# Kernel optimization log

Measured on AMD Instinct MI355X. Metric: run time of the kernel, lower is better.

## Reference

```python
import jax, jax.numpy as jnp
import numpy as np


def setup_inputs() -> dict:
    key = jax.random.key(0)
    k1, k2, k3, k4 = jax.random.split(key, 4)
    B, Cin, H, W = 16, 64, 96, 96
    D, O, KH, KW, S = 100, 256, 3, 3, 3
    x = jax.random.normal(k1, (B, Cin, H, W), dtype=jnp.float32)
    dictionary = jax.random.normal(k2, (D, Cin, KH, KW), dtype=jnp.float32) * 0.05
    lookup_coefficients = jax.random.normal(k3, (O, KH, KW, S), dtype=jnp.float32) * 0.1
    lookup_indices = jax.random.randint(k4, (O, KH, KW, S), 0, D, dtype=jnp.int64)
    return {
        "x": x,
        "dictionary": dictionary,
        "lookup_coefficients": lookup_coefficients,
        "lookup_indices": lookup_indices,
    }


def reference(x, dictionary, lookup_coefficients, lookup_indices):
    # Dense conv with the small dictionary: [B, Cin, H, W] x [D, Cin, kh, kw] -> [B, D, Oh, Ow]
    conv_out = jax.lax.conv_general_dilated(
        x, dictionary,
        window_strides=(1, 1),
        padding=((1, 1), (1, 1)),
        dimension_numbers=("NCHW", "OIHW", "NCHW"),
    )
    O = lookup_coefficients.shape[0]
    D = dictionary.shape[0]
    # Flatten kernel-position and sparsity axes: each (position, slot) contributes
    # coeff * conv_out[:, idx] to output channel o; COO duplicates sum.
    idx = lookup_indices.reshape(O, -1)      # [O, P*S]
    coeff = lookup_coefficients.reshape(O, -1)  # [O, P*S]
    # Scatter-add into a per-output-channel weight over dictionary entries: W[o, d]
    Wmat = jnp.zeros((O, D), dtype=conv_out.dtype).at[jnp.arange(O)[:, None], idx].add(coeff)
    # Gather-weighted-sum == sparse (O x D) matmul against conv_out channels
    out = jnp.einsum("od,bdhw->bohw", Wmat, conv_out)
    return out
```

## Files before the change

kernel.cpp:

```cpp
#include <hip/hip_runtime.h>

#define NB   16
#define CIN  64
#define HH   96
#define WW   96
#define DD   100
#define OO   256
#define NWG  (NB * HH)
#define NCV  1536
#define WPAD 50

typedef __attribute__((ext_vector_type(8))) short  bf16x8;
typedef __attribute__((ext_vector_type(4))) float  f32x4;

#define FSWZ(wp) ((((wp) ^ ((wp) >> 3)) & 7) << 4)

static __device__ __forceinline__ unsigned short f32_to_bf16(float f) {
    unsigned int u = __float_as_uint(f);
    u += 0x7FFFu + ((u >> 16) & 1u);
    return (unsigned short)(u >> 16);
}

__global__ __launch_bounds__(256) void prep_kernel(
    const float* __restrict__ x, const float* __restrict__ dict,
    const float* __restrict__ coeff, const int* __restrict__ idx,
    unsigned short* __restrict__ x2, unsigned short* __restrict__ weff2,
    unsigned short* __restrict__ zbuf)
{
    __shared__ unsigned short lds[CIN * 100];
    __shared__ float wrow[DD];
    const int blk = blockIdx.x, tid = threadIdx.x;

    if (blk < NWG) {
        const int b = blk / HH, h = blk % HH;
        for (int it = 0; it < 6; ++it) {
            int i = tid + it * 256;
            int c = i / 24, w4 = i % 24;
            float4 v = *reinterpret_cast<const float4*>(
                x + (((size_t)(b * CIN + c) * HH + h) * WW + w4 * 4));
            ushort4 u;
            u.x = f32_to_bf16(v.x); u.y = f32_to_bf16(v.y);
            u.z = f32_to_bf16(v.z); u.w = f32_to_bf16(v.w);
            *reinterpret_cast<ushort4*>(&lds[c * 100 + w4 * 4]) = u;
        }
        __syncthreads();
        for (int it = 0; it < 6; ++it) {
            int i = tid + it * 256;
            int w = i / 16, c = (i % 16) * 4;
            ushort4 u;
            u.x = lds[(c + 0) * 100 + w];
            u.y = lds[(c + 1) * 100 + w];
            u.z = lds[(c + 2) * 100 + w];
            u.w = lds[(c + 3) * 100 + w];
            *reinterpret_cast<ushort4*>(x2 + (((size_t)(b * HH + h) * WW + w) * CIN + c)) = u;
        }
    } else {
        const int o = blk - NWG;
        if (o == 0 && tid < 8) zbuf[tid] = 0;
        if (tid < DD) wrow[tid] = 0.f;
        __syncthreads();
        if (tid == 0) {
            for (int s = 0; s < 27; ++s) wrow[idx[o * 27 + s]] += coeff[o * 27 + s];
        }
        __syncthreads();
        for (int j = tid; j < 576; j += 256) {
            int kpos = j >> 6, c = j & 63;
            float s = 0.f;
            for (int d = 0; d < DD; ++d)
                s += wrow[d] * dict[d * 576 + c * 9 + kpos];
            int otile = o >> 4, ks = c >> 5;
            int lane8 = (o & 15) | (((c >> 3) & 3) << 4);
            weff2[((size_t)(kpos * 32 + otile * 2 + ks)) * 512 + lane8 * 8 + (c & 7)]
                = f32_to_bf16(s);
        }
    }
}

__global__ __launch_bounds__(256, 2) void conv_kernel(
    const unsigned short* __restrict__ x2,
    const unsigned short* __restrict__ weff2,
    const unsigned short* __restrict__ zbuf,
    float* __restrict__ out)
{
    __shared__ unsigned short xs[4 * WPAD * 64];

    const int wg  = blockIdx.x;
    const int swz = (wg & 7) * (NCV / 8) + (wg >> 3);
    const int b = swz / 96, rem = swz % 96;
    const int hp = rem >> 1, wh = rem & 1;
    const int h0 = hp * 2, ws = wh * 48;
    const int tid = threadIdx.x;
    const int lane = tid & 63, wn = tid >> 6;
    const int l15 = lane & 15;

    char* xsb = reinterpret_cast<char*>(xs);
    const char* x2b = reinterpret_cast<const char*>(x2) + (size_t)b * HH * WW * 128;
    const char* zbp = reinterpret_cast<const char*>(zbuf);

    const unsigned short* wbase = weff2 + (size_t)(wn * 8) * 512 + lane * 8;
    bf16x8 bfr[4][4];
#pragma unroll
    for (int s = 0; s < 4; ++s) {
        const int off = (s >> 1) * 32 + (s & 1);
#pragma unroll
        for (int n = 0; n < 4; ++n)
            bfr[s][n] = *reinterpret_cast<const bf16x8*>(wbase + (off + n * 2) * 512);
    }

#pragma unroll
    for (int it = 0; it < 7; ++it) {
        int chunk = tid + it * 256;
        if (chunk < 1600) {
            int r = chunk / 400, rem2 = chunk % 400;
            int wp = rem2 >> 3, gb = (rem2 & 7) << 4;
            int hx = h0 - 1 + r, w = ws - 1 + wp;
            const char* src = (w >= 0 && w < WW && hx >= 0 && hx < HH)
                ? x2b + ((size_t)(hx * WW + w) * 128 + (gb ^ FSWZ(wp)))
                : zbp;
            __builtin_amdgcn_global_load_lds(
                (const __attribute__((address_space(1))) void*)src,
                (__attribute__((address_space(3))) void*)(xsb + chunk * 16),
                16, 0, 0);
        }
    }

    f32x4 acc[2][3][4];
#pragma unroll
    for (int q = 0; q < 2; ++q)
#pragma unroll
        for (int m = 0; m < 3; ++m)
#pragma unroll
            for (int n = 0; n < 4; ++n)
                acc[q][m][n] = (f32x4){0.f, 0.f, 0.f, 0.f};

    __syncthreads();

    bf16x8 ax[2][2][3];
    {
        const int cb0 = ((lane >> 4) * 8) * 2;
#pragma unroll
        for (int q = 0; q < 2; ++q)
#pragma unroll
            for (int m = 0; m < 3; ++m) {
                int wpos = m * 16 + l15;
                ax[0][q][m] = *reinterpret_cast<const bf16x8*>(
                    xsb + q * 6400 + wpos * 128 + (cb0 ^ FSWZ(wpos)));
            }
    }

#pragma unroll
    for (int s = 0; s < 18; ++s) {
        if (s < 17) {
            const int s1 = s + 1;
            const int kpos1 = s1 >> 1, ks1 = s1 & 1;
            const int kh1 = kpos1 / 3, dw1 = kpos1 % 3;
            const int cb1 = (ks1 * 32 + (lane >> 4) * 8) * 2;
#pragma unroll
            for (int q = 0; q < 2; ++q)
#pragma unroll
                for (int m = 0; m < 3; ++m) {
                    int wpos = m * 16 + l15 + dw1;
                    ax[s1 & 1][q][m] = *reinterpret_cast<const bf16x8*>(
                        xsb + (kh1 + q) * 6400 + wpos * 128 + (cb1 ^ FSWZ(wpos)));
                }
        }
        __builtin_amdgcn_s_setprio(1);
#pragma unroll
        for (int q = 0; q < 2; ++q)
#pragma unroll
            for (int m = 0; m < 3; ++m)
#pragma unroll
                for (int n = 0; n < 4; ++n)
                    acc[q][m][n] = __builtin_amdgcn_mfma_f32_16x16x32_bf16(
                        ax[s & 1][q][m], bfr[s & 3][n], acc[q][m][n], 0, 0, 0);
        __builtin_amdgcn_s_setprio(0);
        if (s < 14) {
            const int s4 = s + 4;
            const int off = (s4 >> 1) * 32 + (s4 & 1);
#pragma unroll
            for (int n = 0; n < 4; ++n)
                bfr[s & 3][n] = *reinterpret_cast<const bf16x8*>(
                    wbase + (off + n * 2) * 512);
        }
    }

#pragma unroll
    for (int q = 0; q < 2; ++q)
#pragma unroll
        for (int m = 0; m < 3; ++m)
#pragma unroll
            for (int n = 0; n < 4; ++n) {
                int o = wn * 64 + n * 16 + l15;
                int w = ws + m * 16 + (lane >> 4) * 4;
                *reinterpret_cast<f32x4*>(
                    out + (((size_t)(b * OO + o) * HH + h0 + q) * WW + w))
                    = acc[q][m][n];
            }
}

extern "C" void kernel_launch(void* const* d_in, const int* in_sizes, int n_in,
                              void* d_out, int out_size, void* d_ws, size_t ws_size,
                              hipStream_t stream) {
    const float* x     = (const float*)d_in[0];
    const float* dict  = (const float*)d_in[1];
    const float* coeff = (const float*)d_in[2];
    const int*   idx   = (const int*)d_in[3];
    float* out = (float*)d_out;

    char* ws = (char*)d_ws;
    unsigned short* weff2 = (unsigned short*)ws;
    unsigned short* zbuf  = (unsigned short*)(ws + 294912);
    unsigned short* x2    = (unsigned short*)(ws + 1048576);

    prep_kernel<<<NWG + OO, 256, 0, stream>>>(x, dict, coeff, idx, x2, weff2, zbuf);
    conv_kernel<<<NCV, 256, 0, stream>>>(x2, weff2, zbuf, out);
}
```

Baseline: 68.69 us.

## Fuse fp32-to-bf16 input conversion and transpose into conv kernel

Removes the separate prep pass that wrote a bf16 NHWC copy of x to workspace. Each conv workgroup now loads its fp32 rows (with halo) directly, converts them to bf16 into an LDS staging buffer, then transposes into the swizzled channel-last tile. The weight-prep kernel becomes a standalone small launch. This avoids the intermediate global write and re-read, but costs more LDS per block, an extra sync and LDS transpose stage, and duplicated fp32 halo reads.

```diff
diff --git a/kernel.cpp b/kernel.cpp
--- a/kernel.cpp
+++ b/kernel.cpp
@@ -6,9 +6,7 @@
 #define WW   96
 #define DD   100
 #define OO   256
-#define NWG  (NB * HH)
 #define NCV  1536
-#define WPAD 50
 
 typedef __attribute__((ext_vector_type(8))) short  bf16x8;
 typedef __attribute__((ext_vector_type(4))) float  f32x4;
@@ -21,81 +19,50 @@
     return (unsigned short)(u >> 16);
 }
 
-__global__ __launch_bounds__(256) void prep_kernel(
-    const float* __restrict__ x, const float* __restrict__ dict,
-    const float* __restrict__ coeff, const int* __restrict__ idx,
-    unsigned short* __restrict__ x2, unsigned short* __restrict__ weff2,
-    unsigned short* __restrict__ zbuf)
+__global__ __launch_bounds__(256) void weff_prep(
+    const float* __restrict__ dict, const float* __restrict__ coeff,
+    const int* __restrict__ idx, unsigned short* __restrict__ weff2)
 {
-    __shared__ unsigned short lds[CIN * 100];
     __shared__ float wrow[DD];
-    const int blk = blockIdx.x, tid = threadIdx.x;
-
-    if (blk < NWG) {
-        const int b = blk / HH, h = blk % HH;
-        for (int it = 0; it < 6; ++it) {
-            int i = tid + it * 256;
-            int c = i / 24, w4 = i % 24;
-            float4 v = *reinterpret_cast<const float4*>(
-                x + (((size_t)(b * CIN + c) * HH + h) * WW + w4 * 4));
-            ushort4 u;
-            u.x = f32_to_bf16(v.x); u.y = f32_to_bf16(v.y);
-            u.z = f32_to_bf16(v.z); u.w = f32_to_bf16(v.w);
-            *reinterpret_cast<ushort4*>(&lds[c * 100 + w4 * 4]) = u;
-        }
-        __syncthreads();
-        for (int it = 0; it < 6; ++it) {
-            int i = tid + it * 256;
-            int w = i / 16, c = (i % 16) * 4;
-            ushort4 u;
-            u.x = lds[(c + 0) * 100 + w];
-            u.y = lds[(c + 1) * 100 + w];
-            u.z = lds[(c + 2) * 100 + w];
-            u.w = lds[(c + 3) * 100 + w];
-            *reinterpret_cast<ushort4*>(x2 + (((size_t)(b * HH + h) * WW + w) * CIN + c)) = u;
-        }
-    } else {
-        const int o = blk - NWG;
-        if (o == 0 && tid < 8) zbuf[tid] = 0;
-        if (tid < DD) wrow[tid] = 0.f;
-        __syncthreads();
-        if (tid == 0) {
-            for (int s = 0; s < 27; ++s) wrow[idx[o * 27 + s]] += coeff[o * 27 + s];
-        }
-        __syncthreads();
-        for (int j = tid; j < 576; j += 256) {
-            int kpos = j >> 6, c = j & 63;
-            float s = 0.f;
-            for (int d = 0; d < DD; ++d)
-                s += wrow[d] * dict[d * 576 + c * 9 + kpos];
-            int otile = o >> 4, ks = c >> 5;
-            int lane8 = (o & 15) | (((c >> 3) & 3) << 4);
-            weff2[((size_t)(kpos * 32 + otile * 2 + ks)) * 512 + lane8 * 8 + (c & 7)]
-                = f32_to_bf16(s);
-        }
+    const int o = blockIdx.x, tid = threadIdx.x;
+    if (tid < DD) wrow[tid] = 0.f;
+    __syncthreads();
+    if (tid == 0) {
+        for (int s = 0; s < 27; ++s) wrow[idx[o * 27 + s]] += coeff[o * 27 + s];
+    }
+    __syncthreads();
+    for (int j = tid; j < 576; j += 256) {
+        int kpos = j >> 6, c = j & 63;
+        float s = 0.f;
+        for (int d = 0; d < DD; ++d)
+            s += wrow[d] * dict[d * 576 + c * 9 + kpos];
+        int otile = o >> 4, ks = c >> 5;
+        int lane8 = (o & 15) | (((c >> 3) & 3) << 4);
+        weff2[((size_t)(kpos * 32 + otile * 2 + ks)) * 512 + lane8 * 8 + (c & 7)]
+            = f32_to_bf16(s);
     }
 }
 
 __global__ __launch_bounds__(256, 2) void conv_kernel(
-    const unsigned short* __restrict__ x2,
+    const float* __restrict__ x,
     const unsigned short* __restrict__ weff2,
-    const unsigned short* __restrict__ zbuf,
     float* __restrict__ out)
 {
-    __shared__ unsigned short xs[4 * WPAD * 64];
+    __shared__ unsigned short tmp[4 * CIN * 54];
+    __shared__ unsigned short xs[4 * 50 * 64];
 
     const int wg  = blockIdx.x;
     const int swz = (wg & 7) * (NCV / 8) + (wg >> 3);
     const int b = swz / 96, rem = swz % 96;
     const int hp = rem >> 1, wh = rem & 1;
     const int h0 = hp * 2, ws = wh * 48;
+    const int wa = wh ? 44 : 0;
+    const int k0 = wh ? 11 : 0;
     const int tid = threadIdx.x;
     const int lane = tid & 63, wn = tid >> 6;
     const int l15 = lane & 15;
 
     char* xsb = reinterpret_cast<char*>(xs);
-    const char* x2b = reinterpret_cast<const char*>(x2) + (size_t)b * HH * WW * 128;
-    const char* zbp = reinterpret_cast<const char*>(zbuf);
 
     const unsigned short* wbase = weff2 + (size_t)(wn * 8) * 512 + lane * 8;
     bf16x8 bfr[4][4];
@@ -107,20 +74,41 @@
             bfr[s][n] = *reinterpret_cast<const bf16x8*>(wbase + (off + n * 2) * 512);
     }
 
+    const float* xb = x + (size_t)b * CIN * HH * WW;
+#pragma unroll
+    for (int it = 0; it < 13; ++it) {
+        int u = tid + it * 256;
+        int r = u / 832, rem2 = u % 832;
+        int c = rem2 / 13, k = k0 + rem2 % 13;
+        int hx = h0 - 1 + r;
+        float4 v = {0.f, 0.f, 0.f, 0.f};
+        if (hx >= 0 && hx < HH)
+            v = *reinterpret_cast<const float4*>(xb + ((size_t)c * HH + hx) * WW + k * 4);
+        unsigned int lo = (unsigned int)f32_to_bf16(v.x) | ((unsigned int)f32_to_bf16(v.y) << 16);
+        unsigned int hi = (unsigned int)f32_to_bf16(v.z) | ((unsigned int)f32_to_bf16(v.w) << 16);
+        unsigned int* t = reinterpret_cast<unsigned int*>(
+            &tmp[(r * CIN + c) * 54 + (k * 4 - wa)]);
+        t[0] = lo; t[1] = hi;
+    }
+    __syncthreads();
+
 #pragma unroll
     for (int it = 0; it < 7; ++it) {
-        int chunk = tid + it * 256;
-        if (chunk < 1600) {
-            int r = chunk / 400, rem2 = chunk % 400;
-            int wp = rem2 >> 3, gb = (rem2 & 7) << 4;
-            int hx = h0 - 1 + r, w = ws - 1 + wp;
-            const char* src = (w >= 0 && w < WW && hx >= 0 && hx < HH)
-                ? x2b + ((size_t)(hx * WW + w) * 128 + (gb ^ FSWZ(wp)))
-                : zbp;
-            __builtin_amdgcn_global_load_lds(
-                (const __attribute__((address_space(1))) void*)src,
-                (__attribute__((address_space(3))) void*)(xsb + chunk * 16),
-                16, 0, 0);
+        int u = tid + it * 256;
+        if (u < 1600) {
+            int g = u & 7, t2 = u >> 3;
+            int wp = t2 % 50, r = t2 / 50;
+            int c0 = g * 8;
+            int w = ws - 1 + wp;
+            bf16x8 f = {0,0,0,0,0,0,0,0};
+            if (w >= 0 && w < WW) {
+                int wl = w - wa;
+#pragma unroll
+                for (int j = 0; j < 8; ++j)
+                    f[j] = (short)tmp[(r * CIN + c0 + j) * 54 + wl];
+            }
+            *reinterpret_cast<bf16x8*>(
+                xsb + r * 6400 + ((wp * 128 + c0 * 2) ^ FSWZ(wp))) = f;
         }
     }
 
@@ -207,11 +195,8 @@
     const int*   idx   = (const int*)d_in[3];
     float* out = (float*)d_out;
 
-    char* ws = (char*)d_ws;
-    unsigned short* weff2 = (unsigned short*)ws;
-    unsigned short* zbuf  = (unsigned short*)(ws + 294912);
-    unsigned short* x2    = (unsigned short*)(ws + 1048576);
-
-    prep_kernel<<<NWG + OO, 256, 0, stream>>>(x, dict, coeff, idx, x2, weff2, zbuf);
-    conv_kernel<<<NCV, 256, 0, stream>>>(x2, weff2, zbuf, out);
-}
+    unsigned short* weff2 = (unsigned short*)d_ws;
+
+    weff_prep<<<OO, 256, 0, stream>>>(dict, coeff, idx, weff2);
+    conv_kernel<<<NCV, 256, 0, stream>>>(x, weff2, out);
+}
```

New measurement: 79.97 us. +16.4%, slower.
